# Kernel optimization log

Measured on AMD Instinct MI355X. Metric: run time of the kernel, lower is better.

## Reference

```python
import jax, jax.numpy as jnp
import numpy as np

N, S, D = 16, 32, 256      # batch, seq_len, hidden_size
B = 4                      # sample_size (Monte-Carlo beams)
CH = 4 * D                 # cell_hidden_dim = 4*hidden (hard-coded in __init__)
EPS = 1e-20


def _ln(x, g, b):
    m = x.mean(-1, keepdims=True)
    v = ((x - m) ** 2).mean(-1, keepdims=True)
    return (x - m) / jnp.sqrt(v + 1e-5) * g + b


def _masked_softmax(logits, mask):
    p = jax.nn.softmax(logits, axis=-1)
    p = p * mask + EPS
    return p / p.sum(-1, keepdims=True)


def _cell(l, r, w1, b1, w2, b2, ln2_g, ln2_b):
    # TreeLSTM-style fused cell: Linear -> GELU -> Linear -> gates -> LayerNorm
    cat = jnp.concatenate([l, r], axis=-1)                  # (NB, s, 2D)
    inter = jax.nn.gelu(cat @ w1 + b1, approximate=False)   # (NB, s, 4D)
    contents = (inter @ w2 + b2).reshape(*l.shape[:-1], 4, D)
    gates = jax.nn.sigmoid(contents[..., 0:3, :])
    f1, f2, ig = gates[..., 0, :], gates[..., 1, :], gates[..., 2, :]
    parent = contents[..., 3, :]
    return _ln(f1 * l + f2 * r + ig * parent, ln2_g, ln2_b)


def _select(old_h, new_h, mask, accu, dec_W, dec_b, key):
    NB, Sc, Dd = new_h.shape
    old_l, old_r = old_h[:, :-1], old_h[:, 1:]
    nh = new_h * mask[:, :, None]
    pad = jnp.zeros((NB, 1, Dd), nh.dtype)
    l1 = jnp.concatenate([pad, nh[:, :-1]], axis=1)
    l2 = jnp.concatenate([pad, l1[:, :-1]], axis=1)
    r1 = jnp.concatenate([nh[:, 1:], pad], axis=1)
    r2 = jnp.concatenate([r1[:, 1:], pad], axis=1)
    win = jnp.concatenate([l2, l1, nh, r1, r2], axis=-1)    # (NB, Sc, 5D)
    logits = (win @ dec_W + dec_b)[..., 0] / np.sqrt(5 * Dd)
    # straight-through Gumbel softmax (temperature = 1)
    u = jax.random.uniform(key, logits.shape, logits.dtype)
    g = -jnp.log(-jnp.log(u + EPS) + EPS)
    y_soft = _masked_softmax(logits + g, mask)
    y_hard = jax.nn.one_hot(jnp.argmax(y_soft, axis=-1), Sc, dtype=y_soft.dtype)
    sel = jax.lax.stop_gradient(y_hard - y_soft) + y_soft
    soft_scores = jnp.sum(sel * _masked_softmax(logits, mask), axis=1)
    accu = accu + jnp.log(soft_scores + EPS)
    cs = jnp.cumsum(sel, axis=1)
    left = (1.0 - cs)[:, :, None]
    right = (cs - sel)[:, :, None]
    merged = sel[:, :, None] * new_h + left * old_l + right * old_r
    return merged, accu


def setup_inputs() -> dict:
    key = jax.random.key(0)
    ks = jax.random.split(key, 6)
    f32 = jnp.float32
    return {
        "x": jax.random.normal(ks[0], (N, S, D), f32),
        "input_mask": jnp.ones((N, S), f32),
        "word_W": jax.random.normal(ks[1], (D, D), f32) / np.sqrt(D),
        "word_b": jnp.zeros((D,), f32),
        "ln_g": jnp.ones((D,), f32),
        "ln_b": jnp.zeros((D,), f32),
        "w1": jax.random.normal(ks[2], (2 * D, CH), f32) / np.sqrt(2 * D),
        "b1": jnp.zeros((CH,), f32),
        "w2": jax.random.normal(ks[3], (CH, 4 * D), f32) / np.sqrt(CH),
        "b2": jnp.zeros((4 * D,), f32),
        "ln2_g": jnp.ones((D,), f32),
        "ln2_b": jnp.zeros((D,), f32),
        "dec_W": jax.random.normal(ks[4], (5 * D, 1), f32) / np.sqrt(5 * D),
        "dec_b": jnp.zeros((1,), f32),
    }


def reference(x, input_mask, word_W, word_b, ln_g, ln_b, w1, b1, w2, b2,
              ln2_g, ln2_b, dec_W, dec_b):
    state = _ln(x @ word_W + word_b, ln_g, ln_b)                 # (N, S, D)
    state = jnp.repeat(state[:, None], B, axis=1).reshape(N * B, S, D)
    lmask = jnp.repeat(input_mask[:, None], B, axis=1).reshape(N * B, S)
    accu = jnp.zeros((N * B,), state.dtype)
    base = jax.random.key(1234)
    # sequential tree-building recurrence; sequence axis shrinks by 1 each step
    for i in range(S - 1):
        l, r = state[:, :-1], state[:, 1:]
        new_state = _cell(l, r, w1, b1, w2, b2, ln2_g, ln2_b)
        if i < S - 2:
            new_state, new_accu = _select(state, new_state, lmask[:, i + 1:],
                                          accu, dec_W, dec_b,
                                          jax.random.fold_in(base, i))
        else:
            new_accu = accu
        done = lmask[:, i + 1]
        state = done[:, None, None] * new_state + (1.0 - done[:, None, None]) * state[:, :-1]
        accu = done * new_accu + (1.0 - done) * accu
    h = state[:, 0].reshape(N, B, D)
    scores = jax.nn.softmax(accu.reshape(N, B, 1), axis=1)
    return jnp.sum(scores * h, axis=1)                            # (N, D)
```

## Files before the change

kernel.cpp:

```cpp
#include <hip/hip_runtime.h>
#include <cstdint>
#include <cstddef>

namespace {
constexpr int kP0 = 31;
constexpr int kM0 = 496;
}

__device__ float g_state[2][64 * 32 * 256];
__device__ float g_nh[2][64 * kP0 * 256];
__device__ float g_s5[2][64 * kP0 * 5];
__device__ float g_nh0[kM0 * 256];
__device__ float g_s50[kM0 * 5];
__device__ float g_inter0[(size_t)kM0 * 1024];
__device__ float g_cont0[(size_t)kM0 * 1024];
__device__ float g_p1[4][128 * 1024];
__device__ float g_p2[4][128 * 1024];
__device__ float g_accu[64];
__device__ int g_slots[2][128];

__device__ __forceinline__ void tf2x32(uint32_t k0, uint32_t k1, uint32_t x0,
                                       uint32_t x1, uint32_t& o0, uint32_t& o1) {
  uint32_t ks2 = k0 ^ k1 ^ 0x1BD11BDAu;
  x0 += k0; x1 += k1;
#define TF_ROT(v, r) (((v) << (r)) | ((v) >> (32 - (r))))
#define TF_RD(r) { x0 += x1; x1 = TF_ROT(x1, r); x1 ^= x0; }
  TF_RD(13) TF_RD(15) TF_RD(26) TF_RD(6)   x0 += k1;  x1 += ks2 + 1u;
  TF_RD(17) TF_RD(29) TF_RD(16) TF_RD(24)  x0 += ks2; x1 += k0 + 2u;
  TF_RD(13) TF_RD(15) TF_RD(26) TF_RD(6)   x0 += k0;  x1 += k1 + 3u;
  TF_RD(17) TF_RD(29) TF_RD(16) TF_RD(24)  x0 += k1;  x1 += ks2 + 4u;
  TF_RD(13) TF_RD(15) TF_RD(26) TF_RD(6)   x0 += ks2; x1 += k0 + 5u;
  o0 = x0; o1 = x1;
#undef TF_RD
#undef TF_ROT
}

__device__ __forceinline__ float blockSum256(float v, float* red4, int tid) {
#pragma unroll
  for (int o = 32; o > 0; o >>= 1) v += __shfl_down(v, o, 64);
  __syncthreads();
  if ((tid & 63) == 0) red4[tid >> 6] = v;
  __syncthreads();
  return red4[0] + red4[1] + red4[2] + red4[3];
}
__device__ __forceinline__ float waveMax64(float v) {
#pragma unroll
  for (int o = 32; o > 0; o >>= 1) v = fmaxf(v, __shfl_xor(v, o, 64));
  return v;
}
__device__ __forceinline__ float waveSum64(float v) {
#pragma unroll
  for (int o = 32; o > 0; o >>= 1) v += __shfl_xor(v, o, 64);
  return v;
}
__device__ __forceinline__ float geluf(float v) {
  return 0.5f * v * (1.0f + erff(v * 0.70710678118654752440f));
}

__global__ __launch_bounds__(256) void k_embed(const float* __restrict__ x,
                                               const float* __restrict__ wW,
                                               const float* __restrict__ wb,
                                               const float* __restrict__ lng,
                                               const float* __restrict__ lnb) {
  int row = blockIdx.x;
  int d = threadIdx.x;
  __shared__ float xs[256];
  __shared__ float red4[4];
  xs[d] = x[row * 256 + d];
  __syncthreads();
  float acc = wb[d];
  for (int k = 0; k < 256; ++k) acc = fmaf(xs[k], wW[k * 256 + d], acc);
  float mean = blockSum256(acc, red4, d) * (1.0f / 256.0f);
  float cen = acc - mean;
  float var = blockSum256(cen * cen, red4, d) * (1.0f / 256.0f);
  float o = cen / sqrtf(var + 1e-5f) * lng[d] + lnb[d];
  int n = row >> 5, s = row & 31;
#pragma unroll
  for (int bb = 0; bb < 4; ++bb)
    g_state[0][((n * 4 + bb) * 32 + s) * 256 + d] = o;
  if (row == 0 && d < 64) g_accu[d] = 0.0f;
}


__global__ __launch_bounds__(128) void k_g1s(const float* __restrict__ w1,
                                             const float* __restrict__ b1) {
  __shared__ float As[64][20];
  __shared__ float Ws[64][132];
  const int tid = threadIdx.x;
  const int colB = blockIdx.x * 128;
  const int rowB = blockIdx.y * 16;
  const int rg = tid >> 5, cgp = tid & 31;
  const int ar = tid & 15, kq = tid >> 4;
  const int wc = tid & 31, wk = tid >> 5;
  const float* Ab;
  {
    int m = rowB + ar;
    int n = m / 31, j = m - n * 31;
    Ab = g_state[0] + (n * 4) * 8192 + j * 256;
  }
  float acc[4][4] = {};
  for (int c = 0; c < 8; ++c) {
    const int kb = c * 64;
#pragma unroll
    for (int q = 0; q < 2; ++q) {
      int kp = kq * 8 + q * 4;
      float4 a = *(const float4*)&Ab[kb + kp];
      As[kp + 0][ar] = a.x; As[kp + 1][ar] = a.y;
      As[kp + 2][ar] = a.z; As[kp + 3][ar] = a.w;
    }
#pragma unroll
    for (int q = 0; q < 16; ++q) {
      int kk = wk * 16 + q;
      *(float4*)&Ws[kk][wc * 4] =
          *(const float4*)&w1[(size_t)(kb + kk) * 1024 + colB + wc * 4];
    }
    __syncthreads();
#pragma unroll
    for (int kk = 0; kk < 64; ++kk) {
      float4 a4 = *(const float4*)&As[kk][rg * 4];
      float4 w4 = *(const float4*)&Ws[kk][cgp * 4];
      float av[4] = {a4.x, a4.y, a4.z, a4.w};
      float wv[4] = {w4.x, w4.y, w4.z, w4.w};
#pragma unroll
      for (int ri = 0; ri < 4; ++ri)
#pragma unroll
        for (int ci = 0; ci < 4; ++ci)
          acc[ri][ci] = fmaf(av[ri], wv[ci], acc[ri][ci]);
    }
    __syncthreads();
  }
  const int col = colB + cgp * 4;
  float4 bb = *(const float4*)&b1[col];
#pragma unroll
  for (int ri = 0; ri < 4; ++ri) {
    int m = rowB + rg * 4 + ri;
    float4 o;
    o.x = geluf(acc[ri][0] + bb.x); o.y = geluf(acc[ri][1] + bb.y);
    o.z = geluf(acc[ri][2] + bb.z); o.w = geluf(acc[ri][3] + bb.w);
    *(float4*)&g_inter0[(size_t)m * 1024 + col] = o;
  }
}

__global__ __launch_bounds__(128) void k_g2s(const float* __restrict__ w2) {
  __shared__ float As[64][20];
  __shared__ float Ws[64][132];
  const int tid = threadIdx.x;
  const int colB = blockIdx.x * 128;
  const int rowB = blockIdx.y * 16;
  const int rg = tid >> 5, cgp = tid & 31;
  const int ar = tid & 15, kq = tid >> 4;
  const int wc = tid & 31, wk = tid >> 5;
  const float* Ab = g_inter0 + (size_t)(rowB + ar) * 1024;
  float acc[4][4] = {};
  for (int c = 0; c < 16; ++c) {
    const int kb = c * 64;
#pragma unroll
    for (int q = 0; q < 2; ++q) {
      int kp = kq * 8 + q * 4;
      float4 a = *(const float4*)&Ab[kb + kp];
      As[kp + 0][ar] = a.x; As[kp + 1][ar] = a.y;
      As[kp + 2][ar] = a.z; As[kp + 3][ar] = a.w;
    }
#pragma unroll
    for (int q = 0; q < 16; ++q) {
      int kk = wk * 16 + q;
      *(float4*)&Ws[kk][wc * 4] =
          *(const float4*)&w2[(size_t)(kb + kk) * 1024 + colB + wc * 4];
    }
    __syncthreads();
#pragma unroll
    for (int kk = 0; kk < 64; ++kk) {
      float4 a4 = *(const float4*)&As[kk][rg * 4];
      float4 w4 = *(const float4*)&Ws[kk][cgp * 4];
      float av[4] = {a4.x, a4.y, a4.z, a4.w};
      float wv[4] = {w4.x, w4.y, w4.z, w4.w};
#pragma unroll
      for (int ri = 0; ri < 4; ++ri)
#pragma unroll
        for (int ci = 0; ci < 4; ++ci)
          acc[ri][ci] = fmaf(av[ri], wv[ci], acc[ri][ci]);
    }
    __syncthreads();
  }
  const int col = colB + cgp * 4;
#pragma unroll
  for (int ri = 0; ri < 4; ++ri) {
    int m = rowB + rg * 4 + ri;
    float4 o = {acc[ri][0], acc[ri][1], acc[ri][2], acc[ri][3]};
    *(float4*)&g_cont0[(size_t)m * 1024 + col] = o;
  }
}

__device__ __forceinline__ float4 g2t_loadA(int grow, int kpos, const float* __restrict__ b1) {
  size_t g = (size_t)grow * 1024 + kpos;
  float4 p0 = *(const float4*)&g_p1[0][g];
  float4 p1 = *(const float4*)&g_p1[1][g];
  float4 p2 = *(const float4*)&g_p1[2][g];
  float4 p3 = *(const float4*)&g_p1[3][g];
  float4 bb = *(const float4*)&b1[kpos];
  float4 r;
  r.x = geluf(p0.x + p1.x + p2.x + p3.x + bb.x);
  r.y = geluf(p0.y + p1.y + p2.y + p3.y + bb.y);
  r.z = geluf(p0.z + p1.z + p2.z + p3.z + bb.z);
  r.w = geluf(p0.w + p1.w + p2.w + p3.w + bb.w);
  return r;
}

__global__ __launch_bounds__(128) void k_g2t(const float* __restrict__ w2,
                                             const float* __restrict__ b1) {
  __shared__ float As[64][36];
  __shared__ float Ws[64][68];
  const int tid = threadIdx.x;
  const int colB = blockIdx.x * 64;
  const int rowB = blockIdx.y * 32;
  const int Ks = blockIdx.z;
  const int kb0 = Ks * 256;
  const int rg = tid >> 4, cgp = tid & 15;
  const int ar = tid & 31, kq = tid >> 5;
  const int wc = tid & 15, wk = tid >> 4;
  const int grow = rowB + ar;
  float acc[4][4] = {};
  for (int c = 0; c < 4; ++c) {
    const int kb = kb0 + c * 64;
#pragma unroll
    for (int q = 0; q < 4; ++q) {
      int kp = kq * 16 + q * 4;
      float4 a = g2t_loadA(grow, kb + kp, b1);
      As[kp + 0][ar] = a.x; As[kp + 1][ar] = a.y;
      As[kp + 2][ar] = a.z; As[kp + 3][ar] = a.w;
    }
#pragma unroll
    for (int q = 0; q < 8; ++q) {
      int kk = wk * 8 + q;
      *(float4*)&Ws[kk][wc * 4] =
          *(const float4*)&w2[(size_t)(kb + kk) * 1024 + colB + wc * 4];
    }
    __syncthreads();
#pragma unroll
    for (int kk = 0; kk < 64; ++kk) {
      float4 a4 = *(const float4*)&As[kk][rg * 4];
      float4 w4 = *(const float4*)&Ws[kk][cgp * 4];
      float av[4] = {a4.x, a4.y, a4.z, a4.w};
      float wv[4] = {w4.x, w4.y, w4.z, w4.w};
#pragma unroll
      for (int ri = 0; ri < 4; ++ri)
#pragma unroll
        for (int ci = 0; ci < 4; ++ci)
          acc[ri][ci] = fmaf(av[ri], wv[ci], acc[ri][ci]);
    }
    __syncthreads();
  }
  const int col = colB + cgp * 4;
#pragma unroll
  for (int ri = 0; ri < 4; ++ri) {
    int r = rowB + rg * 4 + ri;
    float4 o = {acc[ri][0], acc[ri][1], acc[ri][2], acc[ri][3]};
    *(float4*)&g_p2[Ks][r * 1024 + col] = o;
  }
}

__global__ __launch_bounds__(256) void k_cellfull(const float* __restrict__ imask,
                                                  const float* __restrict__ ln2g,
                                                  const float* __restrict__ ln2b,
                                                  const float* __restrict__ decW,
                                                  const float* __restrict__ b2) {
  int m = blockIdx.x;
  int d = threadIdx.x;
  int n = m / 31, j = m - n * 31;
  const float* st = g_state[0] + (n * 4) * 8192;
  const float* crow = g_cont0 + (size_t)m * 1024;
  float c0 = crow[d] + b2[d];
  float c1 = crow[256 + d] + b2[256 + d];
  float c2 = crow[512 + d] + b2[512 + d];
  float c3 = crow[768 + d] + b2[768 + d];
  float l = st[j * 256 + d];
  float r = st[(j + 1) * 256 + d];
  float f1 = 1.0f / (1.0f + expf(-c0));
  float f2 = 1.0f / (1.0f + expf(-c1));
  float ig = 1.0f / (1.0f + expf(-c2));
  float pre = f1 * l + f2 * r + ig * c3;
  __shared__ float red4[4];
  __shared__ float w5[4][5];
  float mean = blockSum256(pre, red4, d) * (1.0f / 256.0f);
  float cen = pre - mean;
  float var = blockSum256(cen * cen, red4, d) * (1.0f / 256.0f);
  float nh = cen / sqrtf(var + 1e-5f) * ln2g[d] + ln2b[d];
  g_nh0[m * 256 + d] = nh;
  float mv = imask[n * 32 + 1 + j];
  float nhm = nh * mv;
  float pv[5];
#pragma unroll
  for (int t = 0; t < 5; ++t) pv[t] = nhm * decW[t * 256 + d];
#pragma unroll
  for (int t = 0; t < 5; ++t)
#pragma unroll
    for (int o = 32; o > 0; o >>= 1) pv[t] += __shfl_down(pv[t], o, 64);
  __syncthreads();
  if ((d & 63) == 0) {
#pragma unroll
    for (int t = 0; t < 5; ++t) w5[d >> 6][t] = pv[t];
  }
  __syncthreads();
  if (d < 5) g_s50[m * 5 + d] = w5[0][d] + w5[1][d] + w5[2][d] + w5[3][d];
}

__global__ __launch_bounds__(256) void k_cm(
    const float* __restrict__ imask, const float* __restrict__ decW,
    const float* __restrict__ decb, const float* __restrict__ b2,
    const float* __restrict__ ln2g, const float* __restrict__ ln2b,
    const float* __restrict__ w1, int i, int last) {
  const int b = blockIdx.x, grp = blockIdx.y;
  const int tid = threadIdx.x, st = tid, lane = tid & 63, wv = tid >> 6;
  const int Sc = 31 - i;
  const int buf = i & 1;
  const int n32 = (b >> 2) * 32;
  __shared__ float sh_nhf[2][256];
  __shared__ float sh_s5f[2][5];
  __shared__ float sA[3][256];
  __shared__ float red4[4];
  __shared__ float w5s[4][5];
  __shared__ int sh_k;
  __shared__ float sh_sv;
  int slot0 = -1, slot1 = -1;
  if (i > 0) { slot0 = g_slots[buf][2 * b]; slot1 = g_slots[buf][2 * b + 1]; }
  const float* s5Src = (i == 0) ? (g_s50 + (b >> 2) * kP0 * 5) : (g_s5[buf] + b * kP0 * 5);
  const float* nhSrcG = (i == 0) ? (g_nh0 + (size_t)(b >> 2) * kP0 * 256)
                                 : (g_nh[buf] + (size_t)b * kP0 * 256);
  const float* stOld = g_state[buf] + b * 8192;
  float* stNew = g_state[(i + 1) & 1] + b * 8192;
  float* nhDst = g_nh[(i + 1) & 1] + (size_t)b * kP0 * 256;
  float* s5Dst = g_s5[(i + 1) & 1] + b * kP0 * 5;
  float done = imask[n32 + i + 1];

  if (i > 0) {
#pragma unroll 1
    for (int s = 0; s < 2; ++s) {
      int j = (s == 0) ? slot0 : slot1;
      if (j < 0) continue;
      int sr = 2 * b + s;
      float c[4];
#pragma unroll
      for (int q = 0; q < 4; ++q) {
        int g = sr * 1024 + q * 256 + st;
        float v = ((g_p2[0][g] + g_p2[1][g]) + g_p2[2][g]) + g_p2[3][g];
        c[q] = v + b2[q * 256 + st];
      }
      float l = stOld[j * 256 + st];
      float r = stOld[(j + 1) * 256 + st];
      float f1 = 1.0f / (1.0f + expf(-c[0]));
      float f2 = 1.0f / (1.0f + expf(-c[1]));
      float ig = 1.0f / (1.0f + expf(-c[2]));
      float pre = f1 * l + f2 * r + ig * c[3];
      float mean = blockSum256(pre, red4, st) * (1.0f / 256.0f);
      float cen = pre - mean;
      float var = blockSum256(cen * cen, red4, st) * (1.0f / 256.0f);
      float nh = cen / sqrtf(var + 1e-5f) * ln2g[st] + ln2b[st];
      sh_nhf[s][st] = nh;
      float mv = imask[n32 + i + 1 + j];
      float nhm = nh * mv;
      float pv[5];
#pragma unroll
      for (int t = 0; t < 5; ++t) pv[t] = nhm * decW[t * 256 + st];
#pragma unroll
      for (int t = 0; t < 5; ++t) {
        float v = pv[t];
#pragma unroll
        for (int o = 32; o > 0; o >>= 1) v += __shfl_down(v, o, 64);
        pv[t] = v;
      }
      __syncthreads();
      if (lane == 0) {
#pragma unroll
        for (int t = 0; t < 5; ++t) w5s[wv][t] = pv[t];
      }
      __syncthreads();
      if (st < 5) sh_s5f[s][st] = w5s[0][st] + w5s[1][st] + w5s[2][st] + w5s[3][st];
    }
  }
  __syncthreads();

  if (!last && tid < 64) {
    int j = lane;
    bool act = j < Sc;
    float mv = 0.f, lg = 0.f;
    if (act) {
      mv = imask[n32 + i + 1 + j];
      float t5 = decb[0];
      if (j >= 2) {
        int rw = j - 2;
        t5 += (i > 0 && rw == slot0) ? sh_s5f[0][0] : (i > 0 && rw == slot1) ? sh_s5f[1][0] : s5Src[rw * 5 + 0];
      }
      if (j >= 1) {
        int rw = j - 1;
        t5 += (i > 0 && rw == slot0) ? sh_s5f[0][1] : (i > 0 && rw == slot1) ? sh_s5f[1][1] : s5Src[rw * 5 + 1];
      }
      {
        int rw = j;
        t5 += (i > 0 && rw == slot0) ? sh_s5f[0][2] : (i > 0 && rw == slot1) ? sh_s5f[1][2] : s5Src[rw * 5 + 2];
      }
      if (j + 1 < Sc) {
        int rw = j + 1;
        t5 += (i > 0 && rw == slot0) ? sh_s5f[0][3] : (i > 0 && rw == slot1) ? sh_s5f[1][3] : s5Src[rw * 5 + 3];
      }
      if (j + 2 < Sc) {
        int rw = j + 2;
        t5 += (i > 0 && rw == slot0) ? sh_s5f[0][4] : (i > 0 && rw == slot1) ? sh_s5f[1][4] : s5Src[rw * 5 + 4];
      }
      lg = t5 / 35.77708763999664f;
    }
    uint32_t fk0, fk1, o0, o1;
    tf2x32(0u, 1234u, 0u, (uint32_t)i, fk0, fk1);
    uint32_t idx = (uint32_t)(b * Sc + j);
    tf2x32(fk0, fk1, 0u, idx, o0, o1);
    uint32_t bits = o0 ^ o1;
    float u = __uint_as_float((bits >> 9) | 0x3f800000u) - 1.0f;
    float gum = -logf(-logf(u + 1e-20f) + 1e-20f);
    float z = lg + gum;
    float zm = waveMax64(act ? z : -3.0e38f);
    float e = act ? expf(z - zm) : 0.f;
    float p = e / waveSum64(e);
    float y = act ? (p * mv + 1e-20f) : 0.f;
    float ys = y / waveSum64(y);
    float av = act ? ys : -1.f;
    int ai = j;
#pragma unroll
    for (int o = 32; o > 0; o >>= 1) {
      float ov = __shfl_xor(av, o, 64);
      int oi = __shfl_xor(ai, o, 64);
      if (ov > av || (ov == av && oi < ai)) { av = ov; ai = oi; }
    }
    float lm = waveMax64(act ? lg : -3.0e38f);
    float e2 = act ? expf(lg - lm) : 0.f;
    float p2 = e2 / waveSum64(e2);
    float y2 = act ? (p2 * mv + 1e-20f) : 0.f;
    float ps = y2 / waveSum64(y2);
    float ysk = __shfl(ys, ai, 64);
    float psk = __shfl(ps, ai, 64);
    float sv = (1.0f - ysk) + ysk;
    if (j == 0) {
      sh_k = ai;
      sh_sv = sv;
      if (grp == 0) {
        g_accu[b] += done * logf(sv * psk + 1e-20f);
        int s0 = -1, s1 = -1;
        if (done != 0.0f) {
          if (ai >= 1) s0 = ai - 1;
          if (ai <= Sc - 2) s1 = ai;
        }
        g_slots[(i + 1) & 1][2 * b] = s0;
        g_slots[(i + 1) & 1][2 * b + 1] = s1;
      }
    }
  }
  __syncthreads();

  if (last) {
    if (grp == 0 && wv == 0) {
      float4 ol = *(const float4*)&stOld[lane * 4];
      float4 nh4;
      if (slot0 == 0) nh4 = *(const float4*)&sh_nhf[0][lane * 4];
      else if (slot1 == 0) nh4 = *(const float4*)&sh_nhf[1][lane * 4];
      else nh4 = *(const float4*)&nhSrcG[lane * 4];
      float4 o4;
      o4.x = done * nh4.x + (1.0f - done) * ol.x;
      o4.y = done * nh4.y + (1.0f - done) * ol.y;
      o4.z = done * nh4.z + (1.0f - done) * ol.z;
      o4.w = done * nh4.w + (1.0f - done) * ol.w;
      *(float4*)&stNew[lane * 4] = o4;
    }
    return;
  }

  int k = sh_k;
  float sv = sh_sv;
#pragma unroll 1
  for (int rr = 0; rr < 2; ++rr) {
    int jrow = grp * 8 + wv * 2 + rr;
    if (jrow >= Sc) continue;
    float4 ol = *(const float4*)&stOld[jrow * 256 + lane * 4];
    float4 ov4;
    if (done != 0.0f) {
      float4 mg;
      if (jrow < k) {
        mg = ol;
      } else if (jrow == k) {
        float4 nh4 = (i > 0 && k == slot0) ? *(const float4*)&sh_nhf[0][lane * 4]
                   : (i > 0 && k == slot1) ? *(const float4*)&sh_nhf[1][lane * 4]
                   : *(const float4*)&nhSrcG[k * 256 + lane * 4];
        mg.x = sv * nh4.x + (1.0f - sv) * ol.x;
        mg.y = sv * nh4.y + (1.0f - sv) * ol.y;
        mg.z = sv * nh4.z + (1.0f - sv) * ol.z;
        mg.w = sv * nh4.w + (1.0f - sv) * ol.w;
      } else {
        float4 orr = *(const float4*)&stOld[(jrow + 1) * 256 + lane * 4];
        mg.x = (1.0f - sv) * ol.x + sv * orr.x;
        mg.y = (1.0f - sv) * ol.y + sv * orr.y;
        mg.z = (1.0f - sv) * ol.z + sv * orr.z;
        mg.w = (1.0f - sv) * ol.w + sv * orr.w;
      }
      ov4.x = done * mg.x + (1.0f - done) * ol.x;
      ov4.y = done * mg.y + (1.0f - done) * ol.y;
      ov4.z = done * mg.z + (1.0f - done) * ol.z;
      ov4.w = done * mg.w + (1.0f - done) * ol.w;
    } else {
      ov4 = ol;
    }
    *(float4*)&stNew[jrow * 256 + lane * 4] = ov4;
    if (jrow < Sc - 1) {
      int src = (done != 0.0f && jrow > k) ? jrow + 1 : jrow;
      float4 nv = (i > 0 && src == slot0) ? *(const float4*)&sh_nhf[0][lane * 4]
                : (i > 0 && src == slot1) ? *(const float4*)&sh_nhf[1][lane * 4]
                : *(const float4*)&nhSrcG[src * 256 + lane * 4];
      *(float4*)&nhDst[jrow * 256 + lane * 4] = nv;
      float mv2 = imask[n32 + i + 2 + jrow];
      float pv[5];
#pragma unroll
      for (int t = 0; t < 5; ++t) {
        const float* dw = decW + t * 256 + lane * 4;
        pv[t] = (nv.x * dw[0] + nv.y * dw[1] + nv.z * dw[2] + nv.w * dw[3]) * mv2;
      }
#pragma unroll
      for (int t = 0; t < 5; ++t) {
        float v = pv[t];
#pragma unroll
        for (int o = 32; o > 0; o >>= 1) v += __shfl_down(v, o, 64);
        pv[t] = v;
      }
      if (lane == 0) {
#pragma unroll
        for (int t = 0; t < 5; ++t) s5Dst[jrow * 5 + t] = pv[t];
      }
    }
  }

  if (done != 0.0f) {
    __syncthreads();
    {
      int d = st;
      float nhKv = (i > 0 && k == slot0) ? sh_nhf[0][d]
                 : (i > 0 && k == slot1) ? sh_nhf[1][d]
                 : nhSrcG[k * 256 + d];
#pragma unroll
      for (int t = 0; t < 3; ++t) {
        int r = k - 1 + t;
        if (r < 0 || r > Sc - 1) continue;
        float ol = stOld[r * 256 + d];
        float mg;
        if (r < k) mg = ol;
        else if (r == k) mg = sv * nhKv + (1.0f - sv) * ol;
        else mg = (1.0f - sv) * ol + sv * stOld[(r + 1) * 256 + d];
        sA[t][d] = done * mg + (1.0f - done) * ol;
      }
    }
    __syncthreads();
    const int Ks = grp;
    const int has0 = (k >= 1);
    const int has1 = (k <= Sc - 2);
    const int kb0 = Ks * 128;
    const float* A0 = (Ks < 2) ? sA[0] : sA[1];
    const float* A1 = (Ks < 2) ? sA[1] : sA[2];
    const int koff = (Ks < 2) ? kb0 : (kb0 - 256);
    const int col = st * 4;
    float a00 = 0.f, a01 = 0.f, a02 = 0.f, a03 = 0.f;
    float a10 = 0.f, a11 = 0.f, a12 = 0.f, a13 = 0.f;
    for (int kk = 0; kk < 128; ++kk) {
      float4 w = *(const float4*)&w1[(size_t)(kb0 + kk) * 1024 + col];
      float av0 = A0[koff + kk];
      float av1 = A1[koff + kk];
      a00 = fmaf(av0, w.x, a00); a01 = fmaf(av0, w.y, a01);
      a02 = fmaf(av0, w.z, a02); a03 = fmaf(av0, w.w, a03);
      a10 = fmaf(av1, w.x, a10); a11 = fmaf(av1, w.y, a11);
      a12 = fmaf(av1, w.z, a12); a13 = fmaf(av1, w.w, a13);
    }
    if (has0) {
      float4 o = {a00, a01, a02, a03};
      *(float4*)&g_p1[Ks][(2 * b + 0) * 1024 + col] = o;
    }
    if (has1) {
      float4 o = {a10, a11, a12, a13};
      *(float4*)&g_p1[Ks][(2 * b + 1) * 1024 + col] = o;
    }
  }
}

__global__ __launch_bounds__(256) void k_final(float* __restrict__ out) {
  int n = blockIdx.x, d = threadIdx.x;
  float a0 = g_accu[n * 4 + 0], a1 = g_accu[n * 4 + 1];
  float a2 = g_accu[n * 4 + 2], a3 = g_accu[n * 4 + 3];
  float mx = fmaxf(fmaxf(a0, a1), fmaxf(a2, a3));
  float e0 = expf(a0 - mx), e1 = expf(a1 - mx), e2 = expf(a2 - mx), e3 = expf(a3 - mx);
  float ssum = e0 + e1 + e2 + e3;
  const float* st1 = g_state[1];
  float h0 = st1[(n * 4 + 0) * 8192 + d];
  float h1 = st1[(n * 4 + 1) * 8192 + d];
  float h2 = st1[(n * 4 + 2) * 8192 + d];
  float h3 = st1[(n * 4 + 3) * 8192 + d];
  out[n * 256 + d] = (e0 / ssum) * h0 + (e1 / ssum) * h1 + (e2 / ssum) * h2 + (e3 / ssum) * h3;
}

extern "C" void kernel_launch(void* const* d_in, const int* in_sizes, int n_in,
                              void* d_out, int out_size, void* d_ws, size_t ws_size,
                              hipStream_t stream) {
  (void)in_sizes; (void)n_in; (void)d_ws; (void)ws_size; (void)out_size;
  const float* x = (const float*)d_in[0];
  const float* imask = (const float*)d_in[1];
  const float* wW = (const float*)d_in[2];
  const float* wb = (const float*)d_in[3];
  const float* lng = (const float*)d_in[4];
  const float* lnb = (const float*)d_in[5];
  const float* w1 = (const float*)d_in[6];
  const float* b1 = (const float*)d_in[7];
  const float* w2 = (const float*)d_in[8];
  const float* b2 = (const float*)d_in[9];
  const float* ln2g = (const float*)d_in[10];
  const float* ln2b = (const float*)d_in[11];
  const float* decW = (const float*)d_in[12];
  const float* decb = (const float*)d_in[13];
  float* out = (float*)d_out;

  k_embed<<<dim3(512), dim3(256), 0, stream>>>(x, wW, wb, lng, lnb);
  k_g1s<<<dim3(8, 31), dim3(128), 0, stream>>>(w1, b1);
  k_g2s<<<dim3(8, 31), dim3(128), 0, stream>>>(w2);
  k_cellfull<<<dim3(kM0), dim3(256), 0, stream>>>(imask, ln2g, ln2b, decW, b2);
  k_cm<<<dim3(64, 4), dim3(256), 0, stream>>>(imask, decW, decb, b2, ln2g, ln2b, w1, 0, 0);
  for (int i = 1; i <= 30; ++i) {
    k_g2t<<<dim3(16, 4, 4), dim3(128), 0, stream>>>(w2, b1);
    int lastf = (i == 30) ? 1 : 0;
    k_cm<<<dim3(64, lastf ? 1 : 4), dim3(256), 0, stream>>>(imask, decW, decb, b2,
                                                            ln2g, ln2b, w1, i, lastf);
  }
  k_final<<<dim3(16), dim3(256), 0, stream>>>(out);
}
```

Measured before the change: 1.324 ms.

## Fuse per-step GEMM2 and cell/merge kernels with a grid-wide atomic barrier

Each recurrence step used to launch two kernels, a split-K GEMM and a cell/merge kernel. They are now merged into one 512-block kernel: each block computes a 16x64 GEMM2 tile with register prefetch, signals a global counter, spins until all blocks arrive, and then runs the cell/merge body. The merge and w1 partial GEMM are also spread over 8 groups instead of 4, with one row per wave, which doubles the parallelism. This halves the number of launches and the gaps between them. The cost is a spin barrier that assumes all 512 blocks are co-resident and would deadlock otherwise, plus atomic loads for the partial sums.

```diff
diff --git a/kernel.cpp b/kernel.cpp
--- a/kernel.cpp
+++ b/kernel.cpp
@@ -18,6 +18,7 @@
 __device__ float g_p2[4][128 * 1024];
 __device__ float g_accu[64];
 __device__ int g_slots[2][128];
+__device__ unsigned g_ctr[32];
 
 __device__ __forceinline__ void tf2x32(uint32_t k0, uint32_t k1, uint32_t x0,
                                        uint32_t x1, uint32_t& o0, uint32_t& o1) {
@@ -56,6 +57,9 @@
 __device__ __forceinline__ float geluf(float v) {
   return 0.5f * v * (1.0f + erff(v * 0.70710678118654752440f));
 }
+__device__ __forceinline__ float p2ld(const float* p) {
+  return __hip_atomic_load(p, __ATOMIC_RELAXED, __HIP_MEMORY_SCOPE_AGENT);
+}
 
 __global__ __launch_bounds__(256) void k_embed(const float* __restrict__ x,
                                                const float* __restrict__ wW,
@@ -79,6 +83,7 @@
   for (int bb = 0; bb < 4; ++bb)
     g_state[0][((n * 4 + bb) * 32 + s) * 256 + d] = o;
   if (row == 0 && d < 64) g_accu[d] = 0.0f;
+  if (row == 1 && d < 32) g_ctr[d] = 0u;
 }
 
 
@@ -204,59 +209,6 @@
   r.z = geluf(p0.z + p1.z + p2.z + p3.z + bb.z);
   r.w = geluf(p0.w + p1.w + p2.w + p3.w + bb.w);
   return r;
-}
-
-__global__ __launch_bounds__(128) void k_g2t(const float* __restrict__ w2,
-                                             const float* __restrict__ b1) {
-  __shared__ float As[64][36];
-  __shared__ float Ws[64][68];
-  const int tid = threadIdx.x;
-  const int colB = blockIdx.x * 64;
-  const int rowB = blockIdx.y * 32;
-  const int Ks = blockIdx.z;
-  const int kb0 = Ks * 256;
-  const int rg = tid >> 4, cgp = tid & 15;
-  const int ar = tid & 31, kq = tid >> 5;
-  const int wc = tid & 15, wk = tid >> 4;
-  const int grow = rowB + ar;
-  float acc[4][4] = {};
-  for (int c = 0; c < 4; ++c) {
-    const int kb = kb0 + c * 64;
-#pragma unroll
-    for (int q = 0; q < 4; ++q) {
-      int kp = kq * 16 + q * 4;
-      float4 a = g2t_loadA(grow, kb + kp, b1);
-      As[kp + 0][ar] = a.x; As[kp + 1][ar] = a.y;
-      As[kp + 2][ar] = a.z; As[kp + 3][ar] = a.w;
-    }
-#pragma unroll
-    for (int q = 0; q < 8; ++q) {
-      int kk = wk * 8 + q;
-      *(float4*)&Ws[kk][wc * 4] =
-          *(const float4*)&w2[(size_t)(kb + kk) * 1024 + colB + wc * 4];
-    }
-    __syncthreads();
-#pragma unroll
-    for (int kk = 0; kk < 64; ++kk) {
-      float4 a4 = *(const float4*)&As[kk][rg * 4];
-      float4 w4 = *(const float4*)&Ws[kk][cgp * 4];
-      float av[4] = {a4.x, a4.y, a4.z, a4.w};
-      float wv[4] = {w4.x, w4.y, w4.z, w4.w};
-#pragma unroll
-      for (int ri = 0; ri < 4; ++ri)
-#pragma unroll
-        for (int ci = 0; ci < 4; ++ci)
-          acc[ri][ci] = fmaf(av[ri], wv[ci], acc[ri][ci]);
-    }
-    __syncthreads();
-  }
-  const int col = colB + cgp * 4;
-#pragma unroll
-  for (int ri = 0; ri < 4; ++ri) {
-    int r = rowB + rg * 4 + ri;
-    float4 o = {acc[ri][0], acc[ri][1], acc[ri][2], acc[ri][3]};
-    *(float4*)&g_p2[Ks][r * 1024 + col] = o;
-  }
 }
 
 __global__ __launch_bounds__(256) void k_cellfull(const float* __restrict__ imask,
@@ -304,23 +256,19 @@
   if (d < 5) g_s50[m * 5 + d] = w5[0][d] + w5[1][d] + w5[2][d] + w5[3][d];
 }
 
-__global__ __launch_bounds__(256) void k_cm(
+template <int FUSED>
+__device__ __forceinline__ void cm_body(
+    int b, int grp, int tid,
     const float* __restrict__ imask, const float* __restrict__ decW,
     const float* __restrict__ decb, const float* __restrict__ b2,
     const float* __restrict__ ln2g, const float* __restrict__ ln2b,
-    const float* __restrict__ w1, int i, int last) {
-  const int b = blockIdx.x, grp = blockIdx.y;
-  const int tid = threadIdx.x, st = tid, lane = tid & 63, wv = tid >> 6;
+    const float* __restrict__ w1, int i, int last,
+    float (*sh_nhf)[256], float (*sh_s5f)[5], float (*sA)[256],
+    float* red4, float (*w5s)[5], int* sh_k, float* sh_sv) {
+  const int st = tid, lane = tid & 63, wv = tid >> 6;
   const int Sc = 31 - i;
   const int buf = i & 1;
   const int n32 = (b >> 2) * 32;
-  __shared__ float sh_nhf[2][256];
-  __shared__ float sh_s5f[2][5];
-  __shared__ float sA[3][256];
-  __shared__ float red4[4];
-  __shared__ float w5s[4][5];
-  __shared__ int sh_k;
-  __shared__ float sh_sv;
   int slot0 = -1, slot1 = -1;
   if (i > 0) { slot0 = g_slots[buf][2 * b]; slot1 = g_slots[buf][2 * b + 1]; }
   const float* s5Src = (i == 0) ? (g_s50 + (b >> 2) * kP0 * 5) : (g_s5[buf] + b * kP0 * 5);
@@ -342,7 +290,12 @@
 #pragma unroll
       for (int q = 0; q < 4; ++q) {
         int g = sr * 1024 + q * 256 + st;
-        float v = ((g_p2[0][g] + g_p2[1][g]) + g_p2[2][g]) + g_p2[3][g];
+        float v;
+        if (FUSED) {
+          v = ((p2ld(&g_p2[0][g]) + p2ld(&g_p2[1][g])) + p2ld(&g_p2[2][g])) + p2ld(&g_p2[3][g]);
+        } else {
+          v = ((g_p2[0][g] + g_p2[1][g]) + g_p2[2][g]) + g_p2[3][g];
+        }
         c[q] = v + b2[q * 256 + st];
       }
       float l = stOld[j * 256 + st];
@@ -431,15 +384,15 @@
     }
     float lm = waveMax64(act ? lg : -3.0e38f);
     float e2 = act ? expf(lg - lm) : 0.f;
-    float p2 = e2 / waveSum64(e2);
-    float y2 = act ? (p2 * mv + 1e-20f) : 0.f;
+    float p2v = e2 / waveSum64(e2);
+    float y2 = act ? (p2v * mv + 1e-20f) : 0.f;
     float ps = y2 / waveSum64(y2);
     float ysk = __shfl(ys, ai, 64);
     float psk = __shfl(ps, ai, 64);
     float sv = (1.0f - ysk) + ysk;
     if (j == 0) {
-      sh_k = ai;
-      sh_sv = sv;
+      *sh_k = ai;
+      *sh_sv = sv;
       if (grp == 0) {
         g_accu[b] += done * logf(sv * psk + 1e-20f);
         int s0 = -1, s1 = -1;
@@ -471,64 +424,64 @@
     return;
   }
 
-  int k = sh_k;
-  float sv = sh_sv;
-#pragma unroll 1
-  for (int rr = 0; rr < 2; ++rr) {
-    int jrow = grp * 8 + wv * 2 + rr;
-    if (jrow >= Sc) continue;
-    float4 ol = *(const float4*)&stOld[jrow * 256 + lane * 4];
-    float4 ov4;
-    if (done != 0.0f) {
-      float4 mg;
-      if (jrow < k) {
-        mg = ol;
-      } else if (jrow == k) {
-        float4 nh4 = (i > 0 && k == slot0) ? *(const float4*)&sh_nhf[0][lane * 4]
-                   : (i > 0 && k == slot1) ? *(const float4*)&sh_nhf[1][lane * 4]
-                   : *(const float4*)&nhSrcG[k * 256 + lane * 4];
-        mg.x = sv * nh4.x + (1.0f - sv) * ol.x;
-        mg.y = sv * nh4.y + (1.0f - sv) * ol.y;
-        mg.z = sv * nh4.z + (1.0f - sv) * ol.z;
-        mg.w = sv * nh4.w + (1.0f - sv) * ol.w;
+  int k = *sh_k;
+  float sv = *sh_sv;
+  {
+    int jrow = grp * 4 + wv;
+    if (jrow < Sc) {
+      float4 ol = *(const float4*)&stOld[jrow * 256 + lane * 4];
+      float4 ov4;
+      if (done != 0.0f) {
+        float4 mg;
+        if (jrow < k) {
+          mg = ol;
+        } else if (jrow == k) {
+          float4 nh4 = (i > 0 && k == slot0) ? *(const float4*)&sh_nhf[0][lane * 4]
+                     : (i > 0 && k == slot1) ? *(const float4*)&sh_nhf[1][lane * 4]
+                     : *(const float4*)&nhSrcG[k * 256 + lane * 4];
+          mg.x = sv * nh4.x + (1.0f - sv) * ol.x;
+          mg.y = sv * nh4.y + (1.0f - sv) * ol.y;
+          mg.z = sv * nh4.z + (1.0f - sv) * ol.z;
+          mg.w = sv * nh4.w + (1.0f - sv) * ol.w;
+        } else {
+          float4 orr = *(const float4*)&stOld[(jrow + 1) * 256 + lane * 4];
+          mg.x = (1.0f - sv) * ol.x + sv * orr.x;
+          mg.y = (1.0f - sv) * ol.y + sv * orr.y;
+          mg.z = (1.0f - sv) * ol.z + sv * orr.z;
+          mg.w = (1.0f - sv) * ol.w + sv * orr.w;
+        }
+        ov4.x = done * mg.x + (1.0f - done) * ol.x;
+        ov4.y = done * mg.y + (1.0f - done) * ol.y;
+        ov4.z = done * mg.z + (1.0f - done) * ol.z;
+        ov4.w = done * mg.w + (1.0f - done) * ol.w;
       } else {
-        float4 orr = *(const float4*)&stOld[(jrow + 1) * 256 + lane * 4];
-        mg.x = (1.0f - sv) * ol.x + sv * orr.x;
-        mg.y = (1.0f - sv) * ol.y + sv * orr.y;
-        mg.z = (1.0f - sv) * ol.z + sv * orr.z;
-        mg.w = (1.0f - sv) * ol.w + sv * orr.w;
-      }
-      ov4.x = done * mg.x + (1.0f - done) * ol.x;
-      ov4.y = done * mg.y + (1.0f - done) * ol.y;
-      ov4.z = done * mg.z + (1.0f - done) * ol.z;
-      ov4.w = done * mg.w + (1.0f - done) * ol.w;
-    } else {
-      ov4 = ol;
-    }
-    *(float4*)&stNew[jrow * 256 + lane * 4] = ov4;
-    if (jrow < Sc - 1) {
-      int src = (done != 0.0f && jrow > k) ? jrow + 1 : jrow;
-      float4 nv = (i > 0 && src == slot0) ? *(const float4*)&sh_nhf[0][lane * 4]
-                : (i > 0 && src == slot1) ? *(const float4*)&sh_nhf[1][lane * 4]
-                : *(const float4*)&nhSrcG[src * 256 + lane * 4];
-      *(float4*)&nhDst[jrow * 256 + lane * 4] = nv;
-      float mv2 = imask[n32 + i + 2 + jrow];
-      float pv[5];
-#pragma unroll
-      for (int t = 0; t < 5; ++t) {
-        const float* dw = decW + t * 256 + lane * 4;
-        pv[t] = (nv.x * dw[0] + nv.y * dw[1] + nv.z * dw[2] + nv.w * dw[3]) * mv2;
-      }
-#pragma unroll
-      for (int t = 0; t < 5; ++t) {
-        float v = pv[t];
-#pragma unroll
-        for (int o = 32; o > 0; o >>= 1) v += __shfl_down(v, o, 64);
-        pv[t] = v;
-      }
-      if (lane == 0) {
-#pragma unroll
-        for (int t = 0; t < 5; ++t) s5Dst[jrow * 5 + t] = pv[t];
+        ov4 = ol;
+      }
+      *(float4*)&stNew[jrow * 256 + lane * 4] = ov4;
+      if (jrow < Sc - 1) {
+        int src = (done != 0.0f && jrow > k) ? jrow + 1 : jrow;
+        float4 nv = (i > 0 && src == slot0) ? *(const float4*)&sh_nhf[0][lane * 4]
+                  : (i > 0 && src == slot1) ? *(const float4*)&sh_nhf[1][lane * 4]
+                  : *(const float4*)&nhSrcG[src * 256 + lane * 4];
+        *(float4*)&nhDst[jrow * 256 + lane * 4] = nv;
+        float mv2 = imask[n32 + i + 2 + jrow];
+        float pv[5];
+#pragma unroll
+        for (int t = 0; t < 5; ++t) {
+          const float* dw = decW + t * 256 + lane * 4;
+          pv[t] = (nv.x * dw[0] + nv.y * dw[1] + nv.z * dw[2] + nv.w * dw[3]) * mv2;
+        }
+#pragma unroll
+        for (int t = 0; t < 5; ++t) {
+          float v = pv[t];
+#pragma unroll
+          for (int o = 32; o > 0; o >>= 1) v += __shfl_down(v, o, 64);
+          pv[t] = v;
+        }
+        if (lane == 0) {
+#pragma unroll
+          for (int t = 0; t < 5; ++t) s5Dst[jrow * 5 + t] = pv[t];
+        }
       }
     }
   }
@@ -553,34 +506,124 @@
       }
     }
     __syncthreads();
-    const int Ks = grp;
-    const int has0 = (k >= 1);
-    const int has1 = (k <= Sc - 2);
+    const int my = grp >> 2;
+    const int Ks = grp & 3;
+    const int has = (my == 0) ? (k >= 1) : (k <= Sc - 2);
     const int kb0 = Ks * 128;
-    const float* A0 = (Ks < 2) ? sA[0] : sA[1];
-    const float* A1 = (Ks < 2) ? sA[1] : sA[2];
+    const float* A = (my == 0) ? ((Ks < 2) ? sA[0] : sA[1])
+                               : ((Ks < 2) ? sA[1] : sA[2]);
     const int koff = (Ks < 2) ? kb0 : (kb0 - 256);
     const int col = st * 4;
-    float a00 = 0.f, a01 = 0.f, a02 = 0.f, a03 = 0.f;
-    float a10 = 0.f, a11 = 0.f, a12 = 0.f, a13 = 0.f;
+    float a0 = 0.f, a1 = 0.f, a2 = 0.f, a3 = 0.f;
     for (int kk = 0; kk < 128; ++kk) {
       float4 w = *(const float4*)&w1[(size_t)(kb0 + kk) * 1024 + col];
-      float av0 = A0[koff + kk];
-      float av1 = A1[koff + kk];
-      a00 = fmaf(av0, w.x, a00); a01 = fmaf(av0, w.y, a01);
-      a02 = fmaf(av0, w.z, a02); a03 = fmaf(av0, w.w, a03);
-      a10 = fmaf(av1, w.x, a10); a11 = fmaf(av1, w.y, a11);
-      a12 = fmaf(av1, w.z, a12); a13 = fmaf(av1, w.w, a13);
-    }
-    if (has0) {
-      float4 o = {a00, a01, a02, a03};
-      *(float4*)&g_p1[Ks][(2 * b + 0) * 1024 + col] = o;
-    }
-    if (has1) {
-      float4 o = {a10, a11, a12, a13};
-      *(float4*)&g_p1[Ks][(2 * b + 1) * 1024 + col] = o;
-    }
-  }
+      float av = A[koff + kk];
+      a0 = fmaf(av, w.x, a0); a1 = fmaf(av, w.y, a1);
+      a2 = fmaf(av, w.z, a2); a3 = fmaf(av, w.w, a3);
+    }
+    if (has) {
+      float4 o = {a0, a1, a2, a3};
+      *(float4*)&g_p1[Ks][(2 * b + my) * 1024 + col] = o;
+    }
+  }
+}
+
+__global__ __launch_bounds__(256) void k_cm0(
+    const float* __restrict__ imask, const float* __restrict__ decW,
+    const float* __restrict__ decb, const float* __restrict__ b2,
+    const float* __restrict__ ln2g, const float* __restrict__ ln2b,
+    const float* __restrict__ w1) {
+  __shared__ float sh_nhf[2][256];
+  __shared__ float sh_s5f[2][5];
+  __shared__ float sA[3][256];
+  __shared__ float red4[4];
+  __shared__ float w5s[4][5];
+  __shared__ int sh_k;
+  __shared__ float sh_sv;
+  cm_body<0>(blockIdx.x, blockIdx.y, threadIdx.x, imask, decW, decb, b2,
+             ln2g, ln2b, w1, 0, 0, sh_nhf, sh_s5f, sA, red4, w5s, &sh_k, &sh_sv);
+}
+
+__global__ __launch_bounds__(256) void k_step(
+    const float* __restrict__ imask, const float* __restrict__ decW,
+    const float* __restrict__ decb, const float* __restrict__ b1,
+    const float* __restrict__ b2, const float* __restrict__ ln2g,
+    const float* __restrict__ ln2b, const float* __restrict__ w1,
+    const float* __restrict__ w2, int i, int last) {
+  const int L = blockIdx.x;
+  const int tid = threadIdx.x;
+  __shared__ float gAs[64][17];
+  __shared__ float gWs[64][68];
+  __shared__ float sh_nhf[2][256];
+  __shared__ float sh_s5f[2][5];
+  __shared__ float sA[3][256];
+  __shared__ float red4[4];
+  __shared__ float w5s[4][5];
+  __shared__ int sh_k;
+  __shared__ float sh_sv;
+
+  {
+    const int colB = (L & 15) * 64;
+    const int rowT = ((L >> 4) & 7) * 16;
+    const int Ks = L >> 7;
+    const int kb0 = Ks * 256;
+    const int row = tid >> 4, cg = tid & 15;
+    const int ar = tid >> 4, ak = (tid & 15) * 4;
+    const int grow = rowT + ar;
+    float4 aR = g2t_loadA(grow, kb0 + ak, b1);
+    float4 wR[4];
+#pragma unroll
+    for (int q = 0; q < 4; ++q) {
+      int f = tid + q * 256; int kk = f >> 4, c4 = f & 15;
+      wR[q] = *(const float4*)&w2[(size_t)(kb0 + kk) * 1024 + colB + c4 * 4];
+    }
+    float acc[4] = {};
+    for (int c = 0; c < 4; ++c) {
+      gAs[ak + 0][ar] = aR.x; gAs[ak + 1][ar] = aR.y;
+      gAs[ak + 2][ar] = aR.z; gAs[ak + 3][ar] = aR.w;
+#pragma unroll
+      for (int q = 0; q < 4; ++q) {
+        int f = tid + q * 256; int kk = f >> 4, c4 = f & 15;
+        *(float4*)&gWs[kk][c4 * 4] = wR[q];
+      }
+      __syncthreads();
+      if (c < 3) {
+        int kb = kb0 + (c + 1) * 64;
+        aR = g2t_loadA(grow, kb + ak, b1);
+#pragma unroll
+        for (int q = 0; q < 4; ++q) {
+          int f = tid + q * 256; int kk = f >> 4, c4 = f & 15;
+          wR[q] = *(const float4*)&w2[(size_t)(kb + kk) * 1024 + colB + c4 * 4];
+        }
+      }
+#pragma unroll
+      for (int kk = 0; kk < 64; ++kk) {
+        float a = gAs[kk][row];
+        float4 w = *(const float4*)&gWs[kk][cg * 4];
+        acc[0] = fmaf(a, w.x, acc[0]); acc[1] = fmaf(a, w.y, acc[1]);
+        acc[2] = fmaf(a, w.z, acc[2]); acc[3] = fmaf(a, w.w, acc[3]);
+      }
+      __syncthreads();
+    }
+    const int col = colB + cg * 4;
+    float* dst = &g_p2[Ks][(rowT + row) * 1024 + col];
+    __hip_atomic_store(&dst[0], acc[0], __ATOMIC_RELAXED, __HIP_MEMORY_SCOPE_AGENT);
+    __hip_atomic_store(&dst[1], acc[1], __ATOMIC_RELAXED, __HIP_MEMORY_SCOPE_AGENT);
+    __hip_atomic_store(&dst[2], acc[2], __ATOMIC_RELAXED, __HIP_MEMORY_SCOPE_AGENT);
+    __hip_atomic_store(&dst[3], acc[3], __ATOMIC_RELAXED, __HIP_MEMORY_SCOPE_AGENT);
+  }
+
+  __syncthreads();
+  if (tid == 0) {
+    __hip_atomic_fetch_add(&g_ctr[i], 1u, __ATOMIC_RELEASE, __HIP_MEMORY_SCOPE_AGENT);
+    while (__hip_atomic_load(&g_ctr[i], __ATOMIC_RELAXED, __HIP_MEMORY_SCOPE_AGENT) < 512u)
+      __builtin_amdgcn_s_sleep(2);
+    (void)__hip_atomic_load(&g_ctr[i], __ATOMIC_ACQUIRE, __HIP_MEMORY_SCOPE_AGENT);
+  }
+  __syncthreads();
+
+  cm_body<1>(L >> 3, L & 7, tid, imask, decW, decb, b2, ln2g, ln2b, w1, i, last,
+             sh_nhf, sh_s5f, sA, red4, w5s, &sh_k, &sh_sv);
 }
 
 __global__ __launch_bounds__(256) void k_final(float* __restrict__ out) {
@@ -622,12 +665,10 @@
   k_g1s<<<dim3(8, 31), dim3(128), 0, stream>>>(w1, b1);
   k_g2s<<<dim3(8, 31), dim3(128), 0, stream>>>(w2);
   k_cellfull<<<dim3(kM0), dim3(256), 0, stream>>>(imask, ln2g, ln2b, decW, b2);
-  k_cm<<<dim3(64, 4), dim3(256), 0, stream>>>(imask, decW, decb, b2, ln2g, ln2b, w1, 0, 0);
+  k_cm0<<<dim3(64, 8), dim3(256), 0, stream>>>(imask, decW, decb, b2, ln2g, ln2b, w1);
   for (int i = 1; i <= 30; ++i) {
-    k_g2t<<<dim3(16, 4, 4), dim3(128), 0, stream>>>(w2, b1);
-    int lastf = (i == 30) ? 1 : 0;
-    k_cm<<<dim3(64, lastf ? 1 : 4), dim3(256), 0, stream>>>(imask, decW, decb, b2,
-                                                            ln2g, ln2b, w1, i, lastf);
+    k_step<<<dim3(512), dim3(256), 0, stream>>>(imask, decW, decb, b1, b2, ln2g,
+                                                ln2b, w1, w2, i, (i == 30) ? 1 : 0);
   }
   k_final<<<dim3(16), dim3(256), 0, stream>>>(out);
 }
```

New measurement: 2.231 ms. 68.5% more time.

## Spread per-step GEMM and merge work over more blocks with register prefetch

Applied to the files above, without the earlier changes.

The per-step w2 GEMM kernel now uses 16-row tiles with 256 threads, so it launches twice as many blocks, and it prefetches the next A/W tile into registers while the current tile is being computed. Each thread now produces a 1x4 output instead of a 4x4 block. The merge/w1 kernel grid doubles from 4 to 8 y-blocks. Each of its threads handles one state row and one of the two w1 output rows over a half column range, instead of two rows and two outputs. The aim is to raise parallelism in the latency-bound sequential recurrence, at the cost of less register-level reuse and more redundant weight loads.

```diff
diff --git a/kernel.cpp b/kernel.cpp
--- a/kernel.cpp
+++ b/kernel.cpp
@@ -206,57 +206,56 @@
   return r;
 }
 
-__global__ __launch_bounds__(128) void k_g2t(const float* __restrict__ w2,
+__global__ __launch_bounds__(256) void k_g2t(const float* __restrict__ w2,
                                              const float* __restrict__ b1) {
-  __shared__ float As[64][36];
+  __shared__ float As[64][17];
   __shared__ float Ws[64][68];
   const int tid = threadIdx.x;
   const int colB = blockIdx.x * 64;
-  const int rowB = blockIdx.y * 32;
+  const int rowB = blockIdx.y * 16;
   const int Ks = blockIdx.z;
   const int kb0 = Ks * 256;
-  const int rg = tid >> 4, cgp = tid & 15;
-  const int ar = tid & 31, kq = tid >> 5;
-  const int wc = tid & 15, wk = tid >> 4;
+  const int row = tid >> 4, cg = tid & 15;
+  const int ar = tid >> 4, ak = (tid & 15) * 4;
   const int grow = rowB + ar;
-  float acc[4][4] = {};
+  float4 aR = g2t_loadA(grow, kb0 + ak, b1);
+  float4 wR[4];
+#pragma unroll
+  for (int q = 0; q < 4; ++q) {
+    int f = tid + q * 256; int kk = f >> 4, c4 = f & 15;
+    wR[q] = *(const float4*)&w2[(size_t)(kb0 + kk) * 1024 + colB + c4 * 4];
+  }
+  float acc[4] = {};
   for (int c = 0; c < 4; ++c) {
-    const int kb = kb0 + c * 64;
+    As[ak + 0][ar] = aR.x; As[ak + 1][ar] = aR.y;
+    As[ak + 2][ar] = aR.z; As[ak + 3][ar] = aR.w;
 #pragma unroll
     for (int q = 0; q < 4; ++q) {
-      int kp = kq * 16 + q * 4;
-      float4 a = g2t_loadA(grow, kb + kp, b1);
-      As[kp + 0][ar] = a.x; As[kp + 1][ar] = a.y;
-      As[kp + 2][ar] = a.z; As[kp + 3][ar] = a.w;
-    }
-#pragma unroll
-    for (int q = 0; q < 8; ++q) {
-      int kk = wk * 8 + q;
-      *(float4*)&Ws[kk][wc * 4] =
-          *(const float4*)&w2[(size_t)(kb + kk) * 1024 + colB + wc * 4];
-    }
-    __syncthreads();
+      int f = tid + q * 256; int kk = f >> 4, c4 = f & 15;
+      *(float4*)&Ws[kk][c4 * 4] = wR[q];
+    }
+    __syncthreads();
+    if (c < 3) {
+      int kb = kb0 + (c + 1) * 64;
+      aR = g2t_loadA(grow, kb + ak, b1);
+#pragma unroll
+      for (int q = 0; q < 4; ++q) {
+        int f = tid + q * 256; int kk = f >> 4, c4 = f & 15;
+        wR[q] = *(const float4*)&w2[(size_t)(kb + kk) * 1024 + colB + c4 * 4];
+      }
+    }
 #pragma unroll
     for (int kk = 0; kk < 64; ++kk) {
-      float4 a4 = *(const float4*)&As[kk][rg * 4];
-      float4 w4 = *(const float4*)&Ws[kk][cgp * 4];
-      float av[4] = {a4.x, a4.y, a4.z, a4.w};
-      float wv[4] = {w4.x, w4.y, w4.z, w4.w};
-#pragma unroll
-      for (int ri = 0; ri < 4; ++ri)
-#pragma unroll
-        for (int ci = 0; ci < 4; ++ci)
-          acc[ri][ci] = fmaf(av[ri], wv[ci], acc[ri][ci]);
-    }
-    __syncthreads();
-  }
-  const int col = colB + cgp * 4;
-#pragma unroll
-  for (int ri = 0; ri < 4; ++ri) {
-    int r = rowB + rg * 4 + ri;
-    float4 o = {acc[ri][0], acc[ri][1], acc[ri][2], acc[ri][3]};
-    *(float4*)&g_p2[Ks][r * 1024 + col] = o;
-  }
+      float a = As[kk][row];
+      float4 w = *(const float4*)&Ws[kk][cg * 4];
+      acc[0] = fmaf(a, w.x, acc[0]); acc[1] = fmaf(a, w.y, acc[1]);
+      acc[2] = fmaf(a, w.z, acc[2]); acc[3] = fmaf(a, w.w, acc[3]);
+    }
+    __syncthreads();
+  }
+  int col = colB + cg * 4;
+  float4 o = {acc[0], acc[1], acc[2], acc[3]};
+  *(float4*)&g_p2[Ks][(rowB + row) * 1024 + col] = o;
 }
 
 __global__ __launch_bounds__(256) void k_cellfull(const float* __restrict__ imask,
@@ -473,62 +472,62 @@
 
   int k = sh_k;
   float sv = sh_sv;
-#pragma unroll 1
-  for (int rr = 0; rr < 2; ++rr) {
-    int jrow = grp * 8 + wv * 2 + rr;
-    if (jrow >= Sc) continue;
-    float4 ol = *(const float4*)&stOld[jrow * 256 + lane * 4];
-    float4 ov4;
-    if (done != 0.0f) {
-      float4 mg;
-      if (jrow < k) {
-        mg = ol;
-      } else if (jrow == k) {
-        float4 nh4 = (i > 0 && k == slot0) ? *(const float4*)&sh_nhf[0][lane * 4]
-                   : (i > 0 && k == slot1) ? *(const float4*)&sh_nhf[1][lane * 4]
-                   : *(const float4*)&nhSrcG[k * 256 + lane * 4];
-        mg.x = sv * nh4.x + (1.0f - sv) * ol.x;
-        mg.y = sv * nh4.y + (1.0f - sv) * ol.y;
-        mg.z = sv * nh4.z + (1.0f - sv) * ol.z;
-        mg.w = sv * nh4.w + (1.0f - sv) * ol.w;
+  {
+    int jrow = grp * 4 + wv;
+    if (jrow < Sc) {
+      float4 ol = *(const float4*)&stOld[jrow * 256 + lane * 4];
+      float4 ov4;
+      if (done != 0.0f) {
+        float4 mg;
+        if (jrow < k) {
+          mg = ol;
+        } else if (jrow == k) {
+          float4 nh4 = (i > 0 && k == slot0) ? *(const float4*)&sh_nhf[0][lane * 4]
+                     : (i > 0 && k == slot1) ? *(const float4*)&sh_nhf[1][lane * 4]
+                     : *(const float4*)&nhSrcG[k * 256 + lane * 4];
+          mg.x = sv * nh4.x + (1.0f - sv) * ol.x;
+          mg.y = sv * nh4.y + (1.0f - sv) * ol.y;
+          mg.z = sv * nh4.z + (1.0f - sv) * ol.z;
+          mg.w = sv * nh4.w + (1.0f - sv) * ol.w;
+        } else {
+          float4 orr = *(const float4*)&stOld[(jrow + 1) * 256 + lane * 4];
+          mg.x = (1.0f - sv) * ol.x + sv * orr.x;
+          mg.y = (1.0f - sv) * ol.y + sv * orr.y;
+          mg.z = (1.0f - sv) * ol.z + sv * orr.z;
+          mg.w = (1.0f - sv) * ol.w + sv * orr.w;
+        }
+        ov4.x = done * mg.x + (1.0f - done) * ol.x;
+        ov4.y = done * mg.y + (1.0f - done) * ol.y;
+        ov4.z = done * mg.z + (1.0f - done) * ol.z;
+        ov4.w = done * mg.w + (1.0f - done) * ol.w;
       } else {
-        float4 orr = *(const float4*)&stOld[(jrow + 1) * 256 + lane * 4];
-        mg.x = (1.0f - sv) * ol.x + sv * orr.x;
-        mg.y = (1.0f - sv) * ol.y + sv * orr.y;
-        mg.z = (1.0f - sv) * ol.z + sv * orr.z;
-        mg.w = (1.0f - sv) * ol.w + sv * orr.w;
-      }
-      ov4.x = done * mg.x + (1.0f - done) * ol.x;
-      ov4.y = done * mg.y + (1.0f - done) * ol.y;
-      ov4.z = done * mg.z + (1.0f - done) * ol.z;
-      ov4.w = done * mg.w + (1.0f - done) * ol.w;
-    } else {
-      ov4 = ol;
-    }
-    *(float4*)&stNew[jrow * 256 + lane * 4] = ov4;
-    if (jrow < Sc - 1) {
-      int src = (done != 0.0f && jrow > k) ? jrow + 1 : jrow;
-      float4 nv = (i > 0 && src == slot0) ? *(const float4*)&sh_nhf[0][lane * 4]
-                : (i > 0 && src == slot1) ? *(const float4*)&sh_nhf[1][lane * 4]
-                : *(const float4*)&nhSrcG[src * 256 + lane * 4];
-      *(float4*)&nhDst[jrow * 256 + lane * 4] = nv;
-      float mv2 = imask[n32 + i + 2 + jrow];
-      float pv[5];
-#pragma unroll
-      for (int t = 0; t < 5; ++t) {
-        const float* dw = decW + t * 256 + lane * 4;
-        pv[t] = (nv.x * dw[0] + nv.y * dw[1] + nv.z * dw[2] + nv.w * dw[3]) * mv2;
-      }
-#pragma unroll
-      for (int t = 0; t < 5; ++t) {
-        float v = pv[t];
-#pragma unroll
-        for (int o = 32; o > 0; o >>= 1) v += __shfl_down(v, o, 64);
-        pv[t] = v;
-      }
-      if (lane == 0) {
-#pragma unroll
-        for (int t = 0; t < 5; ++t) s5Dst[jrow * 5 + t] = pv[t];
+        ov4 = ol;
+      }
+      *(float4*)&stNew[jrow * 256 + lane * 4] = ov4;
+      if (jrow < Sc - 1) {
+        int src = (done != 0.0f && jrow > k) ? jrow + 1 : jrow;
+        float4 nv = (i > 0 && src == slot0) ? *(const float4*)&sh_nhf[0][lane * 4]
+                  : (i > 0 && src == slot1) ? *(const float4*)&sh_nhf[1][lane * 4]
+                  : *(const float4*)&nhSrcG[src * 256 + lane * 4];
+        *(float4*)&nhDst[jrow * 256 + lane * 4] = nv;
+        float mv2 = imask[n32 + i + 2 + jrow];
+        float pv[5];
+#pragma unroll
+        for (int t = 0; t < 5; ++t) {
+          const float* dw = decW + t * 256 + lane * 4;
+          pv[t] = (nv.x * dw[0] + nv.y * dw[1] + nv.z * dw[2] + nv.w * dw[3]) * mv2;
+        }
+#pragma unroll
+        for (int t = 0; t < 5; ++t) {
+          float v = pv[t];
+#pragma unroll
+          for (int o = 32; o > 0; o >>= 1) v += __shfl_down(v, o, 64);
+          pv[t] = v;
+        }
+        if (lane == 0) {
+#pragma unroll
+          for (int t = 0; t < 5; ++t) s5Dst[jrow * 5 + t] = pv[t];
+        }
       }
     }
   }
@@ -553,32 +552,25 @@
       }
     }
     __syncthreads();
-    const int Ks = grp;
-    const int has0 = (k >= 1);
-    const int has1 = (k <= Sc - 2);
+    const int ch = grp >> 2;
+    const int Ks = grp & 3;
+    const int my = st >> 7;
+    const int has = (my == 0) ? (k >= 1) : (k <= Sc - 2);
     const int kb0 = Ks * 128;
-    const float* A0 = (Ks < 2) ? sA[0] : sA[1];
-    const float* A1 = (Ks < 2) ? sA[1] : sA[2];
+    const float* A = (my == 0) ? ((Ks < 2) ? sA[0] : sA[1])
+                               : ((Ks < 2) ? sA[1] : sA[2]);
     const int koff = (Ks < 2) ? kb0 : (kb0 - 256);
-    const int col = st * 4;
-    float a00 = 0.f, a01 = 0.f, a02 = 0.f, a03 = 0.f;
-    float a10 = 0.f, a11 = 0.f, a12 = 0.f, a13 = 0.f;
+    const int col = ch * 512 + (st & 127) * 4;
+    float a0 = 0.f, a1 = 0.f, a2 = 0.f, a3 = 0.f;
     for (int kk = 0; kk < 128; ++kk) {
       float4 w = *(const float4*)&w1[(size_t)(kb0 + kk) * 1024 + col];
-      float av0 = A0[koff + kk];
-      float av1 = A1[koff + kk];
-      a00 = fmaf(av0, w.x, a00); a01 = fmaf(av0, w.y, a01);
-      a02 = fmaf(av0, w.z, a02); a03 = fmaf(av0, w.w, a03);
-      a10 = fmaf(av1, w.x, a10); a11 = fmaf(av1, w.y, a11);
-      a12 = fmaf(av1, w.z, a12); a13 = fmaf(av1, w.w, a13);
-    }
-    if (has0) {
-      float4 o = {a00, a01, a02, a03};
-      *(float4*)&g_p1[Ks][(2 * b + 0) * 1024 + col] = o;
-    }
-    if (has1) {
-      float4 o = {a10, a11, a12, a13};
-      *(float4*)&g_p1[Ks][(2 * b + 1) * 1024 + col] = o;
+      float av = A[koff + kk];
+      a0 = fmaf(av, w.x, a0); a1 = fmaf(av, w.y, a1);
+      a2 = fmaf(av, w.z, a2); a3 = fmaf(av, w.w, a3);
+    }
+    if (has) {
+      float4 o = {a0, a1, a2, a3};
+      *(float4*)&g_p1[Ks][(2 * b + my) * 1024 + col] = o;
     }
   }
 }
@@ -622,11 +614,11 @@
   k_g1s<<<dim3(8, 31), dim3(128), 0, stream>>>(w1, b1);
   k_g2s<<<dim3(8, 31), dim3(128), 0, stream>>>(w2);
   k_cellfull<<<dim3(kM0), dim3(256), 0, stream>>>(imask, ln2g, ln2b, decW, b2);
-  k_cm<<<dim3(64, 4), dim3(256), 0, stream>>>(imask, decW, decb, b2, ln2g, ln2b, w1, 0, 0);
+  k_cm<<<dim3(64, 8), dim3(256), 0, stream>>>(imask, decW, decb, b2, ln2g, ln2b, w1, 0, 0);
   for (int i = 1; i <= 30; ++i) {
-    k_g2t<<<dim3(16, 4, 4), dim3(128), 0, stream>>>(w2, b1);
+    k_g2t<<<dim3(16, 8, 4), dim3(256), 0, stream>>>(w2, b1);
     int lastf = (i == 30) ? 1 : 0;
-    k_cm<<<dim3(64, lastf ? 1 : 4), dim3(256), 0, stream>>>(imask, decW, decb, b2,
+    k_cm<<<dim3(64, lastf ? 1 : 8), dim3(256), 0, stream>>>(imask, decW, decb, b2,
                                                             ln2g, ln2b, w1, i, lastf);
   }
   k_final<<<dim3(16), dim3(256), 0, stream>>>(out);
```

Result: no change. 1.307 ms (-1.3%).
